# Kernel tuning notes

Hardware: AMD Instinct MI355X
Metric: run time of the kernel (lower is better)

The kernel has to match this reference:

```python
import jax, jax.numpy as jnp
import numpy as np

B, S, D, E, TOP_K = 4, 4096, 2048, 64, 2


def setup_inputs() -> dict:
    key = jax.random.key(0)
    kx, kw, kb = jax.random.split(key, 3)
    x = jax.random.normal(kx, (B, S, D), dtype=jnp.float32)
    # nn.Linear default init: U(-1/sqrt(D), 1/sqrt(D))
    bound = 1.0 / np.sqrt(D)
    W = jax.random.uniform(kw, (D, E), dtype=jnp.float32, minval=-bound, maxval=bound)
    b = jax.random.uniform(kb, (E,), dtype=jnp.float32, minval=-bound, maxval=bound)
    return {"x": x, "W": W, "b": b}


def reference(x, W, b):
    # gate projection: [B,S,D] @ [D,E] -> [B,S,E]
    gates = jnp.einsum("bsd,de->bse", x, W) + b
    # eval path: no noise. top-k over experts, then softmax over the k selected logits
    weights, indices = jax.lax.top_k(gates, TOP_K)  # [B,S,K]
    weights = jax.nn.softmax(weights, axis=-1)
    return weights, indices
```

## Files before the change

### kernel.cpp

```cpp
#include <hip/hip_runtime.h>
#include <math.h>

#define M_TOKENS 16384
#define E_EXPERTS 64
#define K_DIM 2048
#define KSPLIT 4
#define KCHUNK (K_DIM / KSPLIT)
#define ESPLIT 4
#define EPW (E_EXPERTS / ESPLIT)
#define PSTRIDE (KSPLIT * E_EXPERTS)

__global__ __launch_bounds__(256) void gates_kernel(
    const float* __restrict__ x, const float* __restrict__ W,
    float* __restrict__ part) {
  const int tid = threadIdx.x;
  const int lane = tid & 63;
  const int eh = __builtin_amdgcn_readfirstlane(tid >> 6);
  const int tg = blockIdx.x >> 2;
  const int kc = blockIdx.x & 3;
  const int t = tg * 64 + lane;
  const int kbase = kc * KCHUNK;

  const float* xp = x + (size_t)t * K_DIM + kbase;
  const float* wp = W + (size_t)kbase * E_EXPERTS + eh * EPW;

  float acc[EPW];
#pragma unroll
  for (int e = 0; e < EPW; ++e) acc[e] = 0.0f;

  float4 b0 = *reinterpret_cast<const float4*>(xp + 0);
  float4 b1 = *reinterpret_cast<const float4*>(xp + 4);
  float4 b2 = *reinterpret_cast<const float4*>(xp + 8);
  float4 b3 = *reinterpret_cast<const float4*>(xp + 12);

#define FMA4(bv, kofs)                                                        \
  do {                                                                        \
    const float* wr0 = wp + (size_t)(kofs)*E_EXPERTS;                         \
    float xs[4] = {bv.x, bv.y, bv.z, bv.w};                                   \
    _Pragma("unroll") for (int kk = 0; kk < 4; ++kk) {                        \
      const float* wr = wr0 + kk * E_EXPERTS;                                 \
      _Pragma("unroll") for (int e = 0; e < EPW; ++e)                         \
        acc[e] = fmaf(xs[kk], wr[e], acc[e]);                                 \
    }                                                                         \
  } while (0)

  for (int g = 0; g < KCHUNK / 16 - 1; ++g) {
    const int k0 = g * 16;
    FMA4(b0, k0 + 0);  b0 = *reinterpret_cast<const float4*>(xp + k0 + 16);
    FMA4(b1, k0 + 4);  b1 = *reinterpret_cast<const float4*>(xp + k0 + 20);
    FMA4(b2, k0 + 8);  b2 = *reinterpret_cast<const float4*>(xp + k0 + 24);
    FMA4(b3, k0 + 12); b3 = *reinterpret_cast<const float4*>(xp + k0 + 28);
  }
  {
    const int k0 = KCHUNK - 16;
    FMA4(b0, k0 + 0);
    FMA4(b1, k0 + 4);
    FMA4(b2, k0 + 8);
    FMA4(b3, k0 + 12);
  }
#undef FMA4

  float* p = part + (size_t)t * PSTRIDE + kc * E_EXPERTS + eh * EPW;
#pragma unroll
  for (int v = 0; v < EPW / 4; ++v) {
    *reinterpret_cast<float4*>(p + v * 4) =
        make_float4(acc[4 * v + 0], acc[4 * v + 1], acc[4 * v + 2],
                    acc[4 * v + 3]);
  }
}

__global__ __launch_bounds__(64) void reduce_topk_kernel(
    const float* __restrict__ part, const float* __restrict__ bias,
    float* __restrict__ out) {
  const int t = blockIdx.x * 64 + threadIdx.x;
  const float4* p = reinterpret_cast<const float4*>(part + (size_t)t * PSTRIDE);
  const float4* b4 = reinterpret_cast<const float4*>(bias);

  float m1 = -INFINITY, m2 = -INFINITY;
  int i1 = 0, i2 = 0;

#pragma unroll 4
  for (int e4 = 0; e4 < 16; ++e4) {
    float4 a = p[e4];
    float4 b = p[16 + e4];
    float4 c = p[32 + e4];
    float4 d = p[48 + e4];
    float4 bb = b4[e4];
    float g[4];
    g[0] = bb.x + a.x; g[0] += b.x; g[0] += c.x; g[0] += d.x;
    g[1] = bb.y + a.y; g[1] += b.y; g[1] += c.y; g[1] += d.y;
    g[2] = bb.z + a.z; g[2] += b.z; g[2] += c.z; g[2] += d.z;
    g[3] = bb.w + a.w; g[3] += b.w; g[3] += c.w; g[3] += d.w;
#pragma unroll
    for (int j = 0; j < 4; ++j) {
      int e = e4 * 4 + j;
      if (g[j] > m1) {
        m2 = m1; i2 = i1;
        m1 = g[j]; i1 = e;
      } else if (g[j] > m2) {
        m2 = g[j]; i2 = e;
      }
    }
  }

  float w0 = 1.0f / (1.0f + expf(m2 - m1));
  out[2 * t + 0] = w0;
  out[2 * t + 1] = 1.0f - w0;
  float* oidx = out + 2 * (size_t)M_TOKENS;
  oidx[2 * t + 0] = (float)i1;
  oidx[2 * t + 1] = (float)i2;
}

__global__ __launch_bounds__(64) void router_fused_kernel(
    const float* __restrict__ x, const float* __restrict__ W,
    const float* __restrict__ bias, float* __restrict__ out) {
  const int t = blockIdx.x * 64 + threadIdx.x;
  const float* xrow = x + (size_t)t * K_DIM;

  float acc[E_EXPERTS];
#pragma unroll
  for (int e = 0; e < E_EXPERTS; ++e) acc[e] = 0.0f;

  for (int k4 = 0; k4 < K_DIM; k4 += 4) {
    float4 xv = *reinterpret_cast<const float4*>(xrow + k4);
    float xs[4] = {xv.x, xv.y, xv.z, xv.w};
#pragma unroll
    for (int kk = 0; kk < 4; ++kk) {
      const float* wrow = W + (size_t)(k4 + kk) * E_EXPERTS;
#pragma unroll
      for (int e = 0; e < E_EXPERTS; ++e) acc[e] = fmaf(xs[kk], wrow[e], acc[e]);
    }
  }

  float m1 = -INFINITY, m2 = -INFINITY;
  int i1 = 0, i2 = 0;
#pragma unroll
  for (int e = 0; e < E_EXPERTS; ++e) {
    float g = acc[e] + bias[e];
    if (g > m1) {
      m2 = m1; i2 = i1;
      m1 = g; i1 = e;
    } else if (g > m2) {
      m2 = g; i2 = e;
    }
  }

  float w0 = 1.0f / (1.0f + expf(m2 - m1));
  out[2 * t + 0] = w0;
  out[2 * t + 1] = 1.0f - w0;
  float* oidx = out + 2 * (size_t)M_TOKENS;
  oidx[2 * t + 0] = (float)i1;
  oidx[2 * t + 1] = (float)i2;
}

extern "C" void kernel_launch(void* const* d_in, const int* in_sizes, int n_in,
                              void* d_out, int out_size, void* d_ws, size_t ws_size,
                              hipStream_t stream) {
  const float* x = (const float*)d_in[0];
  const float* W = (const float*)d_in[1];
  const float* b = (const float*)d_in[2];
  float* out = (float*)d_out;

  const size_t need = (size_t)M_TOKENS * PSTRIDE * sizeof(float);
  if (ws_size >= need) {
    float* part = (float*)d_ws;
    gates_kernel<<<(M_TOKENS / 64) * KSPLIT, 256, 0, stream>>>(x, W, part);
    reduce_topk_kernel<<<M_TOKENS / 64, 64, 0, stream>>>(part, b, out);
  } else {
    router_fused_kernel<<<M_TOKENS / 64, 64, 0, stream>>>(x, W, b, out);
  }
}
```

Baseline: 85.23 us.

## Stage W tiles in double-buffered LDS and remap lanes to experts

The gate GEMM kernel is restructured so that each lane owns one expert and each wave handles 16 tokens. W is staged through a double-buffered shared-memory tile of 128 k-rows, loaded cooperatively by 512 threads. Each lane reads x rows directly as float4 loads that are uniform across the wave, replacing the previous per-lane scattered W reads from global memory and the per-lane x-row traversal. This is meant to cut redundant W traffic and get wave-wide broadcast reuse of x. The cost is 64KB of LDS per block, which limits occupancy, plus a __syncthreads per stage, and x loads that are scalar-like broadcasts rather than coalesced.

```diff
diff --git a/kernel.cpp b/kernel.cpp
--- a/kernel.cpp
+++ b/kernel.cpp
@@ -6,67 +6,89 @@
 #define K_DIM 2048
 #define KSPLIT 4
 #define KCHUNK (K_DIM / KSPLIT)
-#define ESPLIT 4
-#define EPW (E_EXPERTS / ESPLIT)
 #define PSTRIDE (KSPLIT * E_EXPERTS)
+#define TPW 16
+#define WPB 8
+#define TPB2 (TPW * WPB)
+#define SK 128
+#define NS (KCHUNK / SK)
 
-__global__ __launch_bounds__(256) void gates_kernel(
+__global__ __launch_bounds__(512, 4) void gates_kernel(
     const float* __restrict__ x, const float* __restrict__ W,
     float* __restrict__ part) {
+  __shared__ float wlds[2][SK * E_EXPERTS];
+
   const int tid = threadIdx.x;
   const int lane = tid & 63;
-  const int eh = __builtin_amdgcn_readfirstlane(tid >> 6);
+  const int w = __builtin_amdgcn_readfirstlane(tid >> 6);
   const int tg = blockIdx.x >> 2;
   const int kc = blockIdx.x & 3;
-  const int t = tg * 64 + lane;
   const int kbase = kc * KCHUNK;
+  const int tok0 = tg * TPB2 + w * TPW;
 
-  const float* xp = x + (size_t)t * K_DIM + kbase;
-  const float* wp = W + (size_t)kbase * E_EXPERTS + eh * EPW;
+  const float* xw = x + (size_t)tok0 * K_DIM + kbase;
+  const float* wsrc = W + (size_t)kbase * E_EXPERTS;
 
-  float acc[EPW];
+  float acc[TPW];
 #pragma unroll
-  for (int e = 0; e < EPW; ++e) acc[e] = 0.0f;
+  for (int t = 0; t < TPW; ++t) acc[t] = 0.0f;
 
-  float4 b0 = *reinterpret_cast<const float4*>(xp + 0);
-  float4 b1 = *reinterpret_cast<const float4*>(xp + 4);
-  float4 b2 = *reinterpret_cast<const float4*>(xp + 8);
-  float4 b3 = *reinterpret_cast<const float4*>(xp + 12);
+  float4 stg[4];
 
-#define FMA4(bv, kofs)                                                        \
+#define LOADS(s)                                                              \
   do {                                                                        \
-    const float* wr0 = wp + (size_t)(kofs)*E_EXPERTS;                         \
-    float xs[4] = {bv.x, bv.y, bv.z, bv.w};                                   \
-    _Pragma("unroll") for (int kk = 0; kk < 4; ++kk) {                        \
-      const float* wr = wr0 + kk * E_EXPERTS;                                 \
-      _Pragma("unroll") for (int e = 0; e < EPW; ++e)                         \
-        acc[e] = fmaf(xs[kk], wr[e], acc[e]);                                 \
-    }                                                                         \
+    const float* src = wsrc + (size_t)(s) * SK * E_EXPERTS;                   \
+    _Pragma("unroll") for (int j = 0; j < 4; ++j)                             \
+        stg[j] = *reinterpret_cast<const float4*>(src + (tid + 512 * j) * 4); \
   } while (0)
 
-  for (int g = 0; g < KCHUNK / 16 - 1; ++g) {
-    const int k0 = g * 16;
-    FMA4(b0, k0 + 0);  b0 = *reinterpret_cast<const float4*>(xp + k0 + 16);
-    FMA4(b1, k0 + 4);  b1 = *reinterpret_cast<const float4*>(xp + k0 + 20);
-    FMA4(b2, k0 + 8);  b2 = *reinterpret_cast<const float4*>(xp + k0 + 24);
-    FMA4(b3, k0 + 12); b3 = *reinterpret_cast<const float4*>(xp + k0 + 28);
+#define WRITES(s)                                                             \
+  do {                                                                        \
+    float* dst = wlds[(s) & 1];                                               \
+    _Pragma("unroll") for (int j = 0; j < 4; ++j)                             \
+        *reinterpret_cast<float4*>(dst + (tid + 512 * j) * 4) = stg[j];       \
+  } while (0)
+
+  LOADS(0);
+  WRITES(0);
+
+  for (int s = 0; s < NS; ++s) {
+    if (s + 1 < NS) LOADS(s + 1);
+    __syncthreads();
+
+    const float* wb = wlds[s & 1];
+    const float* xs = xw + s * SK;
+
+    for (int kb = 0; kb < SK; kb += 4) {
+      float wv[4];
+#pragma unroll
+      for (int kk = 0; kk < 4; ++kk)
+        wv[kk] = wb[(kb + kk) * E_EXPERTS + lane];
+#pragma unroll
+      for (int g = 0; g < 2; ++g) {
+        float4 xv[8];
+#pragma unroll
+        for (int t8 = 0; t8 < 8; ++t8)
+          xv[t8] = *reinterpret_cast<const float4*>(
+              xs + (size_t)(g * 8 + t8) * K_DIM + kb);
+#pragma unroll
+        for (int kk = 0; kk < 4; ++kk) {
+#pragma unroll
+          for (int t8 = 0; t8 < 8; ++t8)
+            acc[g * 8 + t8] = fmaf(((const float*)&xv[t8])[kk], wv[kk],
+                                   acc[g * 8 + t8]);
+        }
+      }
+    }
+
+    if (s + 1 < NS) WRITES(s + 1);
   }
-  {
-    const int k0 = KCHUNK - 16;
-    FMA4(b0, k0 + 0);
-    FMA4(b1, k0 + 4);
-    FMA4(b2, k0 + 8);
-    FMA4(b3, k0 + 12);
-  }
-#undef FMA4
+#undef LOADS
+#undef WRITES
 
-  float* p = part + (size_t)t * PSTRIDE + kc * E_EXPERTS + eh * EPW;
+  float* p = part + (size_t)tok0 * PSTRIDE + kc * E_EXPERTS + lane;
 #pragma unroll
-  for (int v = 0; v < EPW / 4; ++v) {
-    *reinterpret_cast<float4*>(p + v * 4) =
-        make_float4(acc[4 * v + 0], acc[4 * v + 1], acc[4 * v + 2],
-                    acc[4 * v + 3]);
-  }
+  for (int t = 0; t < TPW; ++t) p[(size_t)t * PSTRIDE] = acc[t];
 }
 
 __global__ __launch_bounds__(64) void reduce_topk_kernel(
@@ -164,7 +186,7 @@
   const size_t need = (size_t)M_TOKENS * PSTRIDE * sizeof(float);
   if (ws_size >= need) {
     float* part = (float*)d_ws;
-    gates_kernel<<<(M_TOKENS / 64) * KSPLIT, 256, 0, stream>>>(x, W, part);
+    gates_kernel<<<(M_TOKENS / TPB2) * KSPLIT, 512, 0, stream>>>(x, W, part);
     reduce_topk_kernel<<<M_TOKENS / 64, 64, 0, stream>>>(part, b, out);
   } else {
     router_fused_kernel<<<M_TOKENS / 64, 64, 0, stream>>>(x, W, b, out);
```

Result: slower. 216.2 us (+153.7%).

## Stage x tiles through double-buffered transposed LDS with coalesced loads

Applied to the files above, without the earlier changes.

The gates kernel now loads 128-token by 32-k tiles of x cooperatively with coalesced float4 reads, then writes them transposed into a padded, double-buffered shared-memory array. Each wave reads one x value per k from LDS and does 32 experts per thread instead of 16, with two waves splitting the tokens. The goal is to replace strided per-thread row reads of x, which coalesce poorly, with coalesced global traffic, and to halve how often W is re-read per token. In exchange it adds a syncthreads per stage and more accumulator registers, and the transposed LDS writes may cause bank conflicts.

```diff
diff --git a/kernel.cpp b/kernel.cpp
--- a/kernel.cpp
+++ b/kernel.cpp
@@ -6,61 +6,84 @@
 #define K_DIM 2048
 #define KSPLIT 4
 #define KCHUNK (K_DIM / KSPLIT)
-#define ESPLIT 4
-#define EPW (E_EXPERTS / ESPLIT)
 #define PSTRIDE (KSPLIT * E_EXPERTS)
+#define TPB 128
+#define SK 32
+#define NS (KCHUNK / SK)
+#define EPW 32
 
 __global__ __launch_bounds__(256) void gates_kernel(
     const float* __restrict__ x, const float* __restrict__ W,
     float* __restrict__ part) {
+  __shared__ float xT[2][SK][TPB + 1];
+
   const int tid = threadIdx.x;
   const int lane = tid & 63;
-  const int eh = __builtin_amdgcn_readfirstlane(tid >> 6);
+  const int w = tid >> 6;
+  const int th = w & 1;
+  const int eh = w >> 1;
   const int tg = blockIdx.x >> 2;
   const int kc = blockIdx.x & 3;
-  const int t = tg * 64 + lane;
   const int kbase = kc * KCHUNK;
+  const int tok0 = tg * TPB;
+  const int mytok = th * 64 + lane;
 
-  const float* xp = x + (size_t)t * K_DIM + kbase;
-  const float* wp = W + (size_t)kbase * E_EXPERTS + eh * EPW;
+  const float* wb0 = W + (size_t)kbase * E_EXPERTS + eh * EPW;
 
   float acc[EPW];
 #pragma unroll
   for (int e = 0; e < EPW; ++e) acc[e] = 0.0f;
 
-  float4 b0 = *reinterpret_cast<const float4*>(xp + 0);
-  float4 b1 = *reinterpret_cast<const float4*>(xp + 4);
-  float4 b2 = *reinterpret_cast<const float4*>(xp + 8);
-  float4 b3 = *reinterpret_cast<const float4*>(xp + 12);
+  float4 stg[4];
 
-#define FMA4(bv, kofs)                                                        \
+#define LOADS(s)                                                              \
   do {                                                                        \
-    const float* wr0 = wp + (size_t)(kofs)*E_EXPERTS;                         \
-    float xs[4] = {bv.x, bv.y, bv.z, bv.w};                                   \
-    _Pragma("unroll") for (int kk = 0; kk < 4; ++kk) {                        \
-      const float* wr = wr0 + kk * E_EXPERTS;                                 \
-      _Pragma("unroll") for (int e = 0; e < EPW; ++e)                         \
-        acc[e] = fmaf(xs[kk], wr[e], acc[e]);                                 \
+    const float* src = x + (size_t)tok0 * K_DIM + kbase + (s) * SK;           \
+    _Pragma("unroll") for (int j = 0; j < 4; ++j) {                           \
+      int f = tid + 256 * j;                                                  \
+      int row = f >> 3, c4 = f & 7;                                           \
+      stg[j] = *reinterpret_cast<const float4*>(src + (size_t)row * K_DIM +   \
+                                                c4 * 4);                      \
     }                                                                         \
   } while (0)
 
-  for (int g = 0; g < KCHUNK / 16 - 1; ++g) {
-    const int k0 = g * 16;
-    FMA4(b0, k0 + 0);  b0 = *reinterpret_cast<const float4*>(xp + k0 + 16);
-    FMA4(b1, k0 + 4);  b1 = *reinterpret_cast<const float4*>(xp + k0 + 20);
-    FMA4(b2, k0 + 8);  b2 = *reinterpret_cast<const float4*>(xp + k0 + 24);
-    FMA4(b3, k0 + 12); b3 = *reinterpret_cast<const float4*>(xp + k0 + 28);
+#define WRITES(s)                                                             \
+  do {                                                                        \
+    float* dst = &xT[(s) & 1][0][0];                                          \
+    _Pragma("unroll") for (int j = 0; j < 4; ++j) {                           \
+      int f = tid + 256 * j;                                                  \
+      int row = f >> 3, c4 = f & 7;                                           \
+      dst[(c4 * 4 + 0) * (TPB + 1) + row] = stg[j].x;                         \
+      dst[(c4 * 4 + 1) * (TPB + 1) + row] = stg[j].y;                         \
+      dst[(c4 * 4 + 2) * (TPB + 1) + row] = stg[j].z;                         \
+      dst[(c4 * 4 + 3) * (TPB + 1) + row] = stg[j].w;                         \
+    }                                                                         \
+  } while (0)
+
+  LOADS(0);
+  WRITES(0);
+
+  for (int s = 0; s < NS; ++s) {
+    if (s + 1 < NS) LOADS(s + 1);
+    __syncthreads();
+
+    const float* wk = wb0 + (size_t)s * SK * E_EXPERTS;
+    const float* xb = &xT[s & 1][0][0];
+#pragma unroll 8
+    for (int k = 0; k < SK; ++k) {
+      float xk = xb[k * (TPB + 1) + mytok];
+#pragma unroll
+      for (int e = 0; e < EPW; ++e)
+        acc[e] = fmaf(xk, wk[k * E_EXPERTS + e], acc[e]);
+    }
+
+    if (s + 1 < NS) WRITES(s + 1);
   }
-  {
-    const int k0 = KCHUNK - 16;
-    FMA4(b0, k0 + 0);
-    FMA4(b1, k0 + 4);
-    FMA4(b2, k0 + 8);
-    FMA4(b3, k0 + 12);
-  }
-#undef FMA4
+#undef LOADS
+#undef WRITES
 
-  float* p = part + (size_t)t * PSTRIDE + kc * E_EXPERTS + eh * EPW;
+  float* p = part + (size_t)(tok0 + mytok) * PSTRIDE + kc * E_EXPERTS +
+             eh * EPW;
 #pragma unroll
   for (int v = 0; v < EPW / 4; ++v) {
     *reinterpret_cast<float4*>(p + v * 4) =
@@ -164,7 +187,7 @@
   const size_t need = (size_t)M_TOKENS * PSTRIDE * sizeof(float);
   if (ws_size >= need) {
     float* part = (float*)d_ws;
-    gates_kernel<<<(M_TOKENS / 64) * KSPLIT, 256, 0, stream>>>(x, W, part);
+    gates_kernel<<<(M_TOKENS / TPB) * KSPLIT, 256, 0, stream>>>(x, W, part);
     reduce_topk_kernel<<<M_TOKENS / 64, 64, 0, stream>>>(part, b, out);
   } else {
     router_fused_kernel<<<M_TOKENS / 64, 64, 0, stream>>>(x, W, b, out);
```

Result: slower. 272.3 us (+219.5%).
